# Performance work log

Measured on AMD Instinct MI355X. Metric: run time of the kernel, lower is better.

Reference implementation:

```python
import jax, jax.numpy as jnp
import numpy as np

N_NODES = 100000
N_EDGES = 3200000


def _cheb_norm(edge_index, edge_weight, num_nodes):
    # PyG ChebConv.__norm__ with normalization='sym', lambda_max=2.0:
    # L_hat = 2/lambda_max * (I - D^-1/2 A D^-1/2) - I = -D^-1/2 A D^-1/2
    # (the +1 diagonal from get_laplacian and the -1 self-loops cancel),
    # so only the off-diagonal terms -d_i^-1/2 w_ij d_j^-1/2 remain.
    src, dst = edge_index[0], edge_index[1]
    deg = jax.ops.segment_sum(edge_weight, src, num_segments=num_nodes)
    safe = jnp.where(deg > 0, deg, 1.0)
    dis = jnp.where(deg > 0, jax.lax.rsqrt(safe), 0.0)  # deg_inv_sqrt, inf -> 0
    return -dis[src] * edge_weight * dis[dst]


def _cheb_conv(x, src, dst, norm, W, b, num_nodes):
    # W: [K, C_in, C_out]. Chebyshev recurrence Tx_k = 2 L_hat Tx_{k-1} - Tx_{k-2}.
    def prop(h):  # (L_hat h)[dst] += norm_e * h[src]
        return jax.ops.segment_sum(norm[:, None] * h[src], dst, num_segments=num_nodes)

    K = W.shape[0]
    out = x @ W[0]
    if K > 1:
        tx1 = prop(x)
        out = out + tx1 @ W[1]
        if K > 2:
            def step(carry, Wk):
                tx_m2, tx_m1, acc = carry
                tx = 2.0 * prop(tx_m1) - tx_m2
                return (tx_m1, tx, acc + tx @ Wk), None
            (_, _, out), _ = jax.lax.scan(step, (x, tx1, out), W[2:])
    if b is not None:
        out = out + b
    return out


def setup_inputs() -> dict:
    key = jax.random.key(0)
    ks = jax.random.split(key, 12)
    x = jax.random.normal(ks[0], (N_NODES, 2), dtype=jnp.float32)
    edge_index = jax.random.randint(ks[1], (2, N_EDGES), 0, N_NODES, dtype=jnp.int64)
    edge_weight = jax.random.uniform(ks[2], (N_EDGES,), dtype=jnp.float32)
    s = 0.1  # keep activations in a sane range (glorot-ish scale)
    W1 = jax.random.normal(ks[3], (39, 2, 14), dtype=jnp.float32) * s
    b1 = jax.random.normal(ks[4], (14,), dtype=jnp.float32) * s
    W2 = jax.random.normal(ks[5], (43, 14, 20), dtype=jnp.float32) * s
    b2 = jax.random.normal(ks[6], (20,), dtype=jnp.float32) * s
    W3 = jax.random.normal(ks[7], (45, 20, 27), dtype=jnp.float32) * s
    b3 = jax.random.normal(ks[8], (27,), dtype=jnp.float32) * s
    W4 = jax.random.normal(ks[9], (1, 27, 1), dtype=jnp.float32) * s  # K=1, no bias
    return {"x": x, "edge_index": edge_index, "edge_weight": edge_weight,
            "W1": W1, "b1": b1, "W2": W2, "b2": b2, "W3": W3, "b3": b3, "W4": W4}


def reference(x, edge_index, edge_weight, W1, b1, W2, b2, W3, b3, W4):
    src, dst = edge_index[0], edge_index[1]
    norm = _cheb_norm(edge_index, edge_weight, N_NODES)
    h = jax.nn.silu(_cheb_conv(x, src, dst, norm, W1, b1, N_NODES))
    h = jax.nn.silu(_cheb_conv(h, src, dst, norm, W2, b2, N_NODES))
    h = jax.nn.silu(_cheb_conv(h, src, dst, norm, W3, b3, N_NODES))
    h = _cheb_conv(h, src, dst, norm, W4, None, N_NODES)
    return jax.nn.sigmoid(h)
```

## Files before the change

### kernel.cpp

```cpp
#include <hip/hip_runtime.h>
#include <math.h>

#define N_NODES 100000
#define N_EDGES 3200000
#define BS 256
#define CAP_SHIFT 7
#define CAP (1 << CAP_SHIFT)


__global__ void scan_partial_kernel(const int* __restrict__ cnt, int* __restrict__ bsums) {
    __shared__ int lds[256];
    int tid = threadIdx.x;
    int base = blockIdx.x * 1024 + tid * 4;
    int s = 0;
#pragma unroll
    for (int i = 0; i < 4; ++i) s += (base + i < N_NODES) ? cnt[base + i] : 0;
    lds[tid] = s;
    __syncthreads();
    for (int off = 128; off > 0; off >>= 1) {
        if (tid < off) lds[tid] += lds[tid + off];
        __syncthreads();
    }
    if (tid == 0) bsums[blockIdx.x] = lds[0];
}

__global__ void scan_bsums_kernel(int* __restrict__ bsums, int nb, int* __restrict__ total_out) {
    if (threadIdx.x == 0 && blockIdx.x == 0) {
        int acc = 0;
        for (int b = 0; b < nb; ++b) {
            int v = bsums[b];
            bsums[b] = acc;
            acc += v;
        }
        *total_out = acc;
    }
}

__global__ void scan_final_kernel(const int* __restrict__ cnt, const int* __restrict__ bsums,
                                  int* __restrict__ rp) {
    __shared__ int lds[256];
    int tid = threadIdx.x;
    int base = blockIdx.x * 1024 + tid * 4;
    int v[4];
    int ts = 0;
#pragma unroll
    for (int i = 0; i < 4; ++i) {
        v[i] = (base + i < N_NODES) ? cnt[base + i] : 0;
        ts += v[i];
    }
    lds[tid] = ts;
    __syncthreads();
    for (int off = 1; off < 256; off <<= 1) {
        int t = (tid >= off) ? lds[tid - off] : 0;
        __syncthreads();
        lds[tid] += t;
        __syncthreads();
    }
    int run = lds[tid] - ts + bsums[blockIdx.x];
#pragma unroll
    for (int i = 0; i < 4; ++i) {
        if (base + i < N_NODES) rp[base + i] = run;
        run += v[i];
    }
}

__global__ void fill_direct_kernel(const int* __restrict__ src, const int* __restrict__ dst,
                                   int* __restrict__ cnt_s, int* __restrict__ cnt_d,
                                   int* __restrict__ bkt_s, int* __restrict__ bkt_d) {
    int e = blockIdx.x * blockDim.x + threadIdx.x;
    if (e >= N_EDGES) return;
    int s = src[e];
    int d = dst[e];
    int slot_s = atomicAdd(&cnt_s[s], 1);
    bkt_s[((size_t)s << CAP_SHIFT) + slot_s] = e;
    int slot_d = atomicAdd(&cnt_d[d], 1);
    bkt_d[((size_t)d << CAP_SHIFT) + slot_d] = e;
}

__global__ void sort_rows_bucket_kernel(const int* __restrict__ cnt, const int* __restrict__ rp,
                                        const int* __restrict__ bkt, int* __restrict__ sorted) {
    int n = blockIdx.x * blockDim.x + threadIdx.x;
    if (n >= N_NODES) return;
    int c = cnt[n];
    const int* row = bkt + ((size_t)n << CAP_SHIFT);
    int beg = rp[n];
    for (int i = 0; i < c; ++i) {
        int v = row[i];
        int r = 0;
        for (int j = 0; j < c; ++j) r += (row[j] < v);
        sorted[beg + r] = v;
    }
}

__global__ void deg_dis_kernel(const int* __restrict__ rp_src, const int* __restrict__ sorted,
                               const float* __restrict__ w, float* __restrict__ dis) {
#pragma clang fp contract(off)
    {
        int n = blockIdx.x * blockDim.x + threadIdx.x;
        if (n >= N_NODES) return;
        float d = 0.f;
        int beg = rp_src[n], end = rp_src[n + 1];
        for (int j = beg; j < end; ++j) d = d + w[sorted[j]];
        dis[n] = (d > 0.f) ? (1.0f / sqrtf(d)) : 0.f;
    }
}

__global__ void csr_fill_kernel(const int* __restrict__ sorted, const int* __restrict__ src,
                                const int* __restrict__ dst, const float* __restrict__ w,
                                const float* __restrict__ dis, int2* __restrict__ packed) {
#pragma clang fp contract(off)
    {
        int j = blockIdx.x * blockDim.x + threadIdx.x;
        if (j >= N_EDGES) return;
        int e = sorted[j];
        int s = src[e], d = dst[e];
        float cw = ((-dis[s]) * w[e]) * dis[d];
        packed[j] = make_int2(s, __float_as_int(cw));
    }
}


template <int CIN, int COUT, int SIN, int SACC>
__global__ void layer_init_kernel(const float* __restrict__ hin, const float* __restrict__ W0,
                                  float* __restrict__ acc) {
    int t = blockIdx.x * blockDim.x + threadIdx.x;
    if (t >= N_NODES * COUT) return;
    int n = t / COUT, co = t - n * COUT;
    const float* hr = hin + (size_t)n * SIN;
    float m = 0.f;
#pragma unroll
    for (int ci = 0; ci < CIN; ++ci) m = fmaf(hr[ci], W0[ci * COUT + co], m);
    acc[(size_t)n * SACC + co] = m;
}

template <int CIN, int COUT, int SIN, int SACC, int GS, int LANES, int R>
__global__ __launch_bounds__(LANES* R) void prop_mm_kernel(
    const int* __restrict__ rp, const int2* __restrict__ pk, const float* __restrict__ hin,
    const float* __restrict__ prev, const float* __restrict__ Wk, int rec,
    float* __restrict__ tx_out, float* __restrict__ acc) {
#pragma clang fp contract(off)
    {
        __shared__ float tls[R][LANES * GS];
        int r = threadIdx.x / LANES;
        int lane = threadIdx.x - r * LANES;
        int n = blockIdx.x * R + r;
        bool vn = (n < N_NODES);
        if (vn) {
            int c0 = lane * GS;
            float s[GS];
#pragma unroll
            for (int g = 0; g < GS; ++g) s[g] = 0.f;
            int beg = rp[n], end = rp[n + 1];
            int j = beg;
            if constexpr (GS == 4) {
                for (; j + 7 < end; j += 8) {
                    int2 p0 = pk[j];
                    int2 p1 = pk[j + 1];
                    int2 p2 = pk[j + 2];
                    int2 p3 = pk[j + 3];
                    int2 p4 = pk[j + 4];
                    int2 p5 = pk[j + 5];
                    int2 p6 = pk[j + 6];
                    int2 p7 = pk[j + 7];
                    const float4 q0 = *reinterpret_cast<const float4*>(hin + (size_t)p0.x * SIN + c0);
                    const float4 q1 = *reinterpret_cast<const float4*>(hin + (size_t)p1.x * SIN + c0);
                    const float4 q2 = *reinterpret_cast<const float4*>(hin + (size_t)p2.x * SIN + c0);
                    const float4 q3 = *reinterpret_cast<const float4*>(hin + (size_t)p3.x * SIN + c0);
                    const float4 q4 = *reinterpret_cast<const float4*>(hin + (size_t)p4.x * SIN + c0);
                    const float4 q5 = *reinterpret_cast<const float4*>(hin + (size_t)p5.x * SIN + c0);
                    const float4 q6 = *reinterpret_cast<const float4*>(hin + (size_t)p6.x * SIN + c0);
                    const float4 q7 = *reinterpret_cast<const float4*>(hin + (size_t)p7.x * SIN + c0);
                    float w0 = __int_as_float(p0.y), w1 = __int_as_float(p1.y);
                    float w2 = __int_as_float(p2.y), w3 = __int_as_float(p3.y);
                    float w4 = __int_as_float(p4.y), w5 = __int_as_float(p5.y);
                    float w6 = __int_as_float(p6.y), w7 = __int_as_float(p7.y);
                    s[0] = s[0] + (w0 * q0.x); s[1] = s[1] + (w0 * q0.y);
                    s[2] = s[2] + (w0 * q0.z); s[3] = s[3] + (w0 * q0.w);
                    s[0] = s[0] + (w1 * q1.x); s[1] = s[1] + (w1 * q1.y);
                    s[2] = s[2] + (w1 * q1.z); s[3] = s[3] + (w1 * q1.w);
                    s[0] = s[0] + (w2 * q2.x); s[1] = s[1] + (w2 * q2.y);
                    s[2] = s[2] + (w2 * q2.z); s[3] = s[3] + (w2 * q2.w);
                    s[0] = s[0] + (w3 * q3.x); s[1] = s[1] + (w3 * q3.y);
                    s[2] = s[2] + (w3 * q3.z); s[3] = s[3] + (w3 * q3.w);
                    s[0] = s[0] + (w4 * q4.x); s[1] = s[1] + (w4 * q4.y);
                    s[2] = s[2] + (w4 * q4.z); s[3] = s[3] + (w4 * q4.w);
                    s[0] = s[0] + (w5 * q5.x); s[1] = s[1] + (w5 * q5.y);
                    s[2] = s[2] + (w5 * q5.z); s[3] = s[3] + (w5 * q5.w);
                    s[0] = s[0] + (w6 * q6.x); s[1] = s[1] + (w6 * q6.y);
                    s[2] = s[2] + (w6 * q6.z); s[3] = s[3] + (w6 * q6.w);
                    s[0] = s[0] + (w7 * q7.x); s[1] = s[1] + (w7 * q7.y);
                    s[2] = s[2] + (w7 * q7.z); s[3] = s[3] + (w7 * q7.w);
                }
                for (; j + 3 < end; j += 4) {
                    int2 p0 = pk[j];
                    int2 p1 = pk[j + 1];
                    int2 p2 = pk[j + 2];
                    int2 p3 = pk[j + 3];
                    const float4 q0 = *reinterpret_cast<const float4*>(hin + (size_t)p0.x * SIN + c0);
                    const float4 q1 = *reinterpret_cast<const float4*>(hin + (size_t)p1.x * SIN + c0);
                    const float4 q2 = *reinterpret_cast<const float4*>(hin + (size_t)p2.x * SIN + c0);
                    const float4 q3 = *reinterpret_cast<const float4*>(hin + (size_t)p3.x * SIN + c0);
                    float w0 = __int_as_float(p0.y), w1 = __int_as_float(p1.y);
                    float w2 = __int_as_float(p2.y), w3 = __int_as_float(p3.y);
                    s[0] = s[0] + (w0 * q0.x); s[1] = s[1] + (w0 * q0.y);
                    s[2] = s[2] + (w0 * q0.z); s[3] = s[3] + (w0 * q0.w);
                    s[0] = s[0] + (w1 * q1.x); s[1] = s[1] + (w1 * q1.y);
                    s[2] = s[2] + (w1 * q1.z); s[3] = s[3] + (w1 * q1.w);
                    s[0] = s[0] + (w2 * q2.x); s[1] = s[1] + (w2 * q2.y);
                    s[2] = s[2] + (w2 * q2.z); s[3] = s[3] + (w2 * q2.w);
                    s[0] = s[0] + (w3 * q3.x); s[1] = s[1] + (w3 * q3.y);
                    s[2] = s[2] + (w3 * q3.z); s[3] = s[3] + (w3 * q3.w);
                }
                for (; j < end; ++j) {
                    int2 p = pk[j];
                    float w = __int_as_float(p.y);
                    const float4 q = *reinterpret_cast<const float4*>(hin + (size_t)p.x * SIN + c0);
                    s[0] = s[0] + (w * q.x); s[1] = s[1] + (w * q.y);
                    s[2] = s[2] + (w * q.z); s[3] = s[3] + (w * q.w);
                }
            } else {
                for (; j + 7 < end; j += 8) {
                    int2 p0 = pk[j];
                    int2 p1 = pk[j + 1];
                    int2 p2 = pk[j + 2];
                    int2 p3 = pk[j + 3];
                    int2 p4 = pk[j + 4];
                    int2 p5 = pk[j + 5];
                    int2 p6 = pk[j + 6];
                    int2 p7 = pk[j + 7];
                    const float2 q0 = *reinterpret_cast<const float2*>(hin + (size_t)p0.x * SIN + c0);
                    const float2 q1 = *reinterpret_cast<const float2*>(hin + (size_t)p1.x * SIN + c0);
                    const float2 q2 = *reinterpret_cast<const float2*>(hin + (size_t)p2.x * SIN + c0);
                    const float2 q3 = *reinterpret_cast<const float2*>(hin + (size_t)p3.x * SIN + c0);
                    const float2 q4 = *reinterpret_cast<const float2*>(hin + (size_t)p4.x * SIN + c0);
                    const float2 q5 = *reinterpret_cast<const float2*>(hin + (size_t)p5.x * SIN + c0);
                    const float2 q6 = *reinterpret_cast<const float2*>(hin + (size_t)p6.x * SIN + c0);
                    const float2 q7 = *reinterpret_cast<const float2*>(hin + (size_t)p7.x * SIN + c0);
                    float w0 = __int_as_float(p0.y), w1 = __int_as_float(p1.y);
                    float w2 = __int_as_float(p2.y), w3 = __int_as_float(p3.y);
                    float w4 = __int_as_float(p4.y), w5 = __int_as_float(p5.y);
                    float w6 = __int_as_float(p6.y), w7 = __int_as_float(p7.y);
                    s[0] = s[0] + (w0 * q0.x); s[1] = s[1] + (w0 * q0.y);
                    s[0] = s[0] + (w1 * q1.x); s[1] = s[1] + (w1 * q1.y);
                    s[0] = s[0] + (w2 * q2.x); s[1] = s[1] + (w2 * q2.y);
                    s[0] = s[0] + (w3 * q3.x); s[1] = s[1] + (w3 * q3.y);
                    s[0] = s[0] + (w4 * q4.x); s[1] = s[1] + (w4 * q4.y);
                    s[0] = s[0] + (w5 * q5.x); s[1] = s[1] + (w5 * q5.y);
                    s[0] = s[0] + (w6 * q6.x); s[1] = s[1] + (w6 * q6.y);
                    s[0] = s[0] + (w7 * q7.x); s[1] = s[1] + (w7 * q7.y);
                }
                for (; j + 3 < end; j += 4) {
                    int2 p0 = pk[j];
                    int2 p1 = pk[j + 1];
                    int2 p2 = pk[j + 2];
                    int2 p3 = pk[j + 3];
                    const float2 q0 = *reinterpret_cast<const float2*>(hin + (size_t)p0.x * SIN + c0);
                    const float2 q1 = *reinterpret_cast<const float2*>(hin + (size_t)p1.x * SIN + c0);
                    const float2 q2 = *reinterpret_cast<const float2*>(hin + (size_t)p2.x * SIN + c0);
                    const float2 q3 = *reinterpret_cast<const float2*>(hin + (size_t)p3.x * SIN + c0);
                    float w0 = __int_as_float(p0.y), w1 = __int_as_float(p1.y);
                    float w2 = __int_as_float(p2.y), w3 = __int_as_float(p3.y);
                    s[0] = s[0] + (w0 * q0.x); s[1] = s[1] + (w0 * q0.y);
                    s[0] = s[0] + (w1 * q1.x); s[1] = s[1] + (w1 * q1.y);
                    s[0] = s[0] + (w2 * q2.x); s[1] = s[1] + (w2 * q2.y);
                    s[0] = s[0] + (w3 * q3.x); s[1] = s[1] + (w3 * q3.y);
                }
                for (; j < end; ++j) {
                    int2 p = pk[j];
                    float w = __int_as_float(p.y);
                    const float2 q = *reinterpret_cast<const float2*>(hin + (size_t)p.x * SIN + c0);
                    s[0] = s[0] + (w * q.x); s[1] = s[1] + (w * q.y);
                }
            }
            float t[GS];
            if (rec) {
#pragma unroll
                for (int g = 0; g < GS; ++g) t[g] = 2.f * s[g] - prev[(size_t)n * SIN + c0 + g];
            } else {
#pragma unroll
                for (int g = 0; g < GS; ++g) t[g] = s[g];
            }
#pragma unroll
            for (int g = 0; g < GS; ++g) tls[r][c0 + g] = t[g];
            if constexpr (GS == 4) {
                *reinterpret_cast<float4*>(tx_out + (size_t)n * SIN + c0) =
                    make_float4(t[0], t[1], t[2], t[3]);
            } else {
                *reinterpret_cast<float2*>(tx_out + (size_t)n * SIN + c0) =
                    make_float2(t[0], t[1]);
            }
        }
        __syncthreads();
        if (vn) {
            for (int co = lane; co < COUT; co += LANES) {
                float m = 0.f;
#pragma unroll
                for (int ci = 0; ci < CIN; ++ci) m = fmaf(tls[r][ci], Wk[ci * COUT + co], m);
                acc[(size_t)n * SACC + co] = acc[(size_t)n * SACC + co] + m;
            }
        }
    }
}

template <int C, int S>
__global__ void silu_bias_kernel(float* __restrict__ a, const float* __restrict__ b) {
#pragma clang fp contract(off)
    {
        int t = blockIdx.x * blockDim.x + threadIdx.x;
        if (t >= N_NODES * C) return;
        int n = t / C, c = t - n * C;
        float x = a[(size_t)n * S + c] + b[c];
        float sig = 1.f / (1.f + expf(-x));
        a[(size_t)n * S + c] = x * sig;
    }
}

__global__ void final_kernel(const float* __restrict__ h, const float* __restrict__ W4,
                             float* __restrict__ out) {
#pragma clang fp contract(off)
    {
        int n = blockIdx.x * blockDim.x + threadIdx.x;
        if (n >= N_NODES) return;
        const float* hr = h + (size_t)n * 28;
        float m = 0.f;
#pragma unroll
        for (int ci = 0; ci < 27; ++ci) m = fmaf(hr[ci], W4[ci], m);
        out[n] = 1.f / (1.f + expf(-m));
    }
}

__global__ void signal_kernel(float* __restrict__ out, float val) {
    int n = blockIdx.x * blockDim.x + threadIdx.x;
    if (n < N_NODES) out[n] = val;
}


static void run_scan(const int* cnt, int* bsums, int* rp, hipStream_t stream) {
    const int nb = (N_NODES + 1023) / 1024;
    scan_partial_kernel<<<nb, 256, 0, stream>>>(cnt, bsums);
    scan_bsums_kernel<<<1, 64, 0, stream>>>(bsums, nb, rp + N_NODES);
    scan_final_kernel<<<nb, 256, 0, stream>>>(cnt, bsums, rp);
}

template <int CIN, int COUT, int SIN, int SACC, int GS, int LANES, int R>
static void run_layer(int K, const float* hin, const float* W, float* acc, float* b0, float* b1,
                      float* b2, const int* rp, const int2* pk, hipStream_t stream) {
    const int gInit = (N_NODES * COUT + BS - 1) / BS;
    const int gProp = (N_NODES + R - 1) / R;
    layer_init_kernel<CIN, COUT, SIN, SACC><<<gInit, BS, 0, stream>>>(hin, W, acc);
    if (K > 1) {
        float* bufs[3] = {b0, b1, b2};
        prop_mm_kernel<CIN, COUT, SIN, SACC, GS, LANES, R><<<gProp, LANES * R, 0, stream>>>(
            rp, pk, hin, nullptr, W + 1 * CIN * COUT, 0, bufs[0], acc);
        const float* pm2 = hin;
        const float* pm1 = bufs[0];
        for (int k = 2; k < K; ++k) {
            float* outb = bufs[(k - 1) % 3];
            prop_mm_kernel<CIN, COUT, SIN, SACC, GS, LANES, R><<<gProp, LANES * R, 0, stream>>>(
                rp, pk, pm1, pm2, W + k * CIN * COUT, 1, outb, acc);
            pm2 = pm1;
            pm1 = outb;
        }
    }
}

extern "C" void kernel_launch(void* const* d_in, const int* in_sizes, int n_in, void* d_out,
                              int out_size, void* d_ws, size_t ws_size, hipStream_t stream) {
    const float* x  = (const float*)d_in[0];
    const int* idx  = (const int*)d_in[1];
    const float* ew = (const float*)d_in[2];
    const float* W1 = (const float*)d_in[3];
    const float* b1 = (const float*)d_in[4];
    const float* W2 = (const float*)d_in[5];
    const float* b2 = (const float*)d_in[6];
    const float* W3 = (const float*)d_in[7];
    const float* b3 = (const float*)d_in[8];
    const float* W4 = (const float*)d_in[9];
    float* out = (float*)d_out;
    (void)in_sizes; (void)n_in; (void)out_size;

    const int* src = idx;
    const int* dst = idx + N_EDGES;

    size_t off = 0;
    auto alloc = [&](size_t bytes) {
        size_t o = off;
        off = (off + bytes + 255) & ~(size_t)255;
        return o;
    };
    char* ws = (char*)d_ws;
    int*   cnt_s   = (int*)(ws + alloc(N_NODES * 4));
    int*   cnt_d   = (int*)(ws + alloc(N_NODES * 4));
    int*   rp_src  = (int*)(ws + alloc((N_NODES + 1) * 4));
    int*   rp_dst  = (int*)(ws + alloc((N_NODES + 1) * 4));
    float* dis     = (float*)(ws + alloc(N_NODES * 4));
    int*   bsums   = (int*)(ws + alloc(512));
    int2*  packed  = (int2*)(ws + alloc((size_t)N_EDGES * 8));
    const size_t pool_off = alloc(0);
    float* t0      = (float*)(ws + alloc((size_t)N_NODES * 20 * 4));
    float* t1      = (float*)(ws + alloc((size_t)N_NODES * 20 * 4));
    float* t2      = (float*)(ws + alloc((size_t)N_NODES * 20 * 4));
    float* accA    = (float*)(ws + alloc((size_t)N_NODES * 16 * 4));
    float* accB    = (float*)(ws + alloc((size_t)N_NODES * 20 * 4));
    float* accC    = (float*)(ws + alloc((size_t)N_NODES * 28 * 4));
    int*   bkt_s   = (int*)(ws + alloc((size_t)N_NODES * CAP * 4));
    int*   bkt_d   = (int*)(ws + alloc((size_t)N_NODES * CAP * 4));
    const size_t NEED = off;
    char* pool = ws + pool_off;
    int* sorted_s = (int*)(pool);
    int* sorted_d = (int*)(pool + ((size_t)16 << 20));

    int gE = (N_EDGES + BS - 1) / BS;
    int gN = (N_NODES + BS - 1) / BS;

    if (ws_size < NEED) {
        signal_kernel<<<gN, BS, 0, stream>>>(
            out, 6000.0f + (float)(ws_size / (1024.0 * 1024.0)));
        return;
    }

    (void)hipMemsetAsync(cnt_s, 0, N_NODES * 4, stream);
    (void)hipMemsetAsync(cnt_d, 0, N_NODES * 4, stream);
    fill_direct_kernel<<<gE, BS, 0, stream>>>(src, dst, cnt_s, cnt_d, bkt_s, bkt_d);
    run_scan(cnt_s, bsums, rp_src, stream);
    run_scan(cnt_d, bsums, rp_dst, stream);
    sort_rows_bucket_kernel<<<gN, BS, 0, stream>>>(cnt_s, rp_src, bkt_s, sorted_s);
    deg_dis_kernel<<<gN, BS, 0, stream>>>(rp_src, sorted_s, ew, dis);
    sort_rows_bucket_kernel<<<gN, BS, 0, stream>>>(cnt_d, rp_dst, bkt_d, sorted_d);
    csr_fill_kernel<<<gE, BS, 0, stream>>>(sorted_d, src, dst, ew, dis, packed);

    run_layer<2, 14, 2, 16, 2, 1, 256>(39, x, W1, accA, t0, t1, t2, rp_dst, packed, stream);
    silu_bias_kernel<14, 16><<<(N_NODES * 14 + BS - 1) / BS, BS, 0, stream>>>(accA, b1);
    run_layer<14, 20, 16, 20, 4, 4, 64>(43, accA, W2, accB, t0, t1, t2, rp_dst, packed, stream);
    silu_bias_kernel<20, 20><<<(N_NODES * 20 + BS - 1) / BS, BS, 0, stream>>>(accB, b2);
    run_layer<20, 27, 20, 28, 4, 5, 51>(45, accB, W3, accC, t0, t1, t2, rp_dst, packed, stream);
    silu_bias_kernel<27, 28><<<(N_NODES * 27 + BS - 1) / BS, BS, 0, stream>>>(accC, b3);
    final_kernel<<<gN, BS, 0, stream>>>(accC, W4, out);
}
```

Measured before the change: 8.148 ms.

## Fuse bucket sort with degree and CSR packing, sort rows in LDS, fuse final SiLU

Merges the per-row bucket sort with the degree/rsqrt computation and with the CSR pack step, so the intermediate sorted edge arrays are no longer written and reread. Each row (up to 64 entries) is copied into shared memory and rank-sorted there instead of repeatedly reading global memory. Rows longer than 64 fall back to a slow in-place rank search. The last bias+SiLU is folded into the final sigmoid kernel, removing one pass over the 28-wide buffer. Blocks shrink to 64 threads with large shared arrays, which may limit occupancy.

```diff
diff --git a/kernel.cpp b/kernel.cpp
--- a/kernel.cpp
+++ b/kernel.cpp
@@ -77,45 +77,89 @@
     bkt_d[((size_t)d << CAP_SHIFT) + slot_d] = e;
 }
 
-__global__ void sort_rows_bucket_kernel(const int* __restrict__ cnt, const int* __restrict__ rp,
-                                        const int* __restrict__ bkt, int* __restrict__ sorted) {
-    int n = blockIdx.x * blockDim.x + threadIdx.x;
-    if (n >= N_NODES) return;
-    int c = cnt[n];
-    const int* row = bkt + ((size_t)n << CAP_SHIFT);
-    int beg = rp[n];
-    for (int i = 0; i < c; ++i) {
-        int v = row[i];
-        int r = 0;
-        for (int j = 0; j < c; ++j) r += (row[j] < v);
-        sorted[beg + r] = v;
-    }
-}
-
-__global__ void deg_dis_kernel(const int* __restrict__ rp_src, const int* __restrict__ sorted,
-                               const float* __restrict__ w, float* __restrict__ dis) {
+__global__ __launch_bounds__(64) void sort_deg_dis_kernel(
+    const int* __restrict__ cnt, const int* __restrict__ bkt,
+    const float* __restrict__ w, float* __restrict__ dis) {
 #pragma clang fp contract(off)
     {
-        int n = blockIdx.x * blockDim.x + threadIdx.x;
+        __shared__ int lr[64][65];
+        __shared__ int ls[64][65];
+        int n = blockIdx.x * 64 + threadIdx.x;
         if (n >= N_NODES) return;
+        int c = cnt[n];
+        const int* row = bkt + ((size_t)n << CAP_SHIFT);
         float d = 0.f;
-        int beg = rp_src[n], end = rp_src[n + 1];
-        for (int j = beg; j < end; ++j) d = d + w[sorted[j]];
+        if (c <= 64) {
+            int* a = lr[threadIdx.x];
+            int* b = ls[threadIdx.x];
+            for (int i = 0; i < c; ++i) a[i] = row[i];
+            for (int i = 0; i < c; ++i) {
+                int v = a[i];
+                int rk = 0;
+                for (int j = 0; j < c; ++j) rk += (a[j] < v);
+                b[rk] = v;
+            }
+            for (int r = 0; r < c; ++r) d = d + w[b[r]];
+        } else {
+            for (int r = 0; r < c; ++r) {
+                for (int i = 0; i < c; ++i) {
+                    int v = row[i];
+                    int rk = 0;
+                    for (int j = 0; j < c; ++j) rk += (row[j] < v);
+                    if (rk == r) { d = d + w[v]; break; }
+                }
+            }
+        }
         dis[n] = (d > 0.f) ? (1.0f / sqrtf(d)) : 0.f;
     }
 }
 
-__global__ void csr_fill_kernel(const int* __restrict__ sorted, const int* __restrict__ src,
-                                const int* __restrict__ dst, const float* __restrict__ w,
-                                const float* __restrict__ dis, int2* __restrict__ packed) {
+__global__ __launch_bounds__(64) void sort_pack_kernel(
+    const int* __restrict__ cnt, const int* __restrict__ rp,
+    const int* __restrict__ bkt, const int* __restrict__ src,
+    const float* __restrict__ w, const float* __restrict__ dis,
+    int2* __restrict__ packed) {
 #pragma clang fp contract(off)
     {
-        int j = blockIdx.x * blockDim.x + threadIdx.x;
-        if (j >= N_EDGES) return;
-        int e = sorted[j];
-        int s = src[e], d = dst[e];
-        float cw = ((-dis[s]) * w[e]) * dis[d];
-        packed[j] = make_int2(s, __float_as_int(cw));
+        __shared__ int lr[64][65];
+        __shared__ int ls[64][65];
+        int n = blockIdx.x * 64 + threadIdx.x;
+        if (n >= N_NODES) return;
+        int c = cnt[n];
+        const int* row = bkt + ((size_t)n << CAP_SHIFT);
+        int beg = rp[n];
+        float din = dis[n];
+        if (c <= 64) {
+            int* a = lr[threadIdx.x];
+            int* b = ls[threadIdx.x];
+            for (int i = 0; i < c; ++i) a[i] = row[i];
+            for (int i = 0; i < c; ++i) {
+                int v = a[i];
+                int rk = 0;
+                for (int j = 0; j < c; ++j) rk += (a[j] < v);
+                b[rk] = v;
+            }
+            for (int r = 0; r < c; ++r) {
+                int e = b[r];
+                int s = src[e];
+                float cw = ((-dis[s]) * w[e]) * din;
+                packed[beg + r] = make_int2(s, __float_as_int(cw));
+            }
+        } else {
+            for (int r = 0; r < c; ++r) {
+                for (int i = 0; i < c; ++i) {
+                    int v = row[i];
+                    int rk = 0;
+                    for (int j = 0; j < c; ++j) rk += (row[j] < v);
+                    if (rk == r) {
+                        int s = src[v];
+                        float cw = ((-dis[s]) * w[v]) * din;
+                        packed[beg + r] = make_int2(s, __float_as_int(cw));
+                        break;
+                    }
+                }
+            }
+        }
     }
 }
 
@@ -315,16 +359,20 @@
     }
 }
 
-__global__ void final_kernel(const float* __restrict__ h, const float* __restrict__ W4,
-                             float* __restrict__ out) {
+__global__ void final_kernel(const float* __restrict__ acc, const float* __restrict__ b3,
+                             const float* __restrict__ W4, float* __restrict__ out) {
 #pragma clang fp contract(off)
     {
         int n = blockIdx.x * blockDim.x + threadIdx.x;
         if (n >= N_NODES) return;
-        const float* hr = h + (size_t)n * 28;
         float m = 0.f;
 #pragma unroll
-        for (int ci = 0; ci < 27; ++ci) m = fmaf(hr[ci], W4[ci], m);
+        for (int ci = 0; ci < 27; ++ci) {
+            float xv = acc[(size_t)n * 28 + ci] + b3[ci];
+            float sig = 1.f / (1.f + expf(-xv));
+            float hv = xv * sig;
+            m = fmaf(hv, W4[ci], m);
+        }
         out[n] = 1.f / (1.f + expf(-m));
     }
 }
@@ -396,7 +444,6 @@
     float* dis     = (float*)(ws + alloc(N_NODES * 4));
     int*   bsums   = (int*)(ws + alloc(512));
     int2*  packed  = (int2*)(ws + alloc((size_t)N_EDGES * 8));
-    const size_t pool_off = alloc(0);
     float* t0      = (float*)(ws + alloc((size_t)N_NODES * 20 * 4));
     float* t1      = (float*)(ws + alloc((size_t)N_NODES * 20 * 4));
     float* t2      = (float*)(ws + alloc((size_t)N_NODES * 20 * 4));
@@ -406,12 +453,10 @@
     int*   bkt_s   = (int*)(ws + alloc((size_t)N_NODES * CAP * 4));
     int*   bkt_d   = (int*)(ws + alloc((size_t)N_NODES * CAP * 4));
     const size_t NEED = off;
-    char* pool = ws + pool_off;
-    int* sorted_s = (int*)(pool);
-    int* sorted_d = (int*)(pool + ((size_t)16 << 20));
 
     int gE = (N_EDGES + BS - 1) / BS;
     int gN = (N_NODES + BS - 1) / BS;
+    const int gSort = (N_NODES + 63) / 64;
 
     if (ws_size < NEED) {
         signal_kernel<<<gN, BS, 0, stream>>>(
@@ -424,16 +469,13 @@
     fill_direct_kernel<<<gE, BS, 0, stream>>>(src, dst, cnt_s, cnt_d, bkt_s, bkt_d);
     run_scan(cnt_s, bsums, rp_src, stream);
     run_scan(cnt_d, bsums, rp_dst, stream);
-    sort_rows_bucket_kernel<<<gN, BS, 0, stream>>>(cnt_s, rp_src, bkt_s, sorted_s);
-    deg_dis_kernel<<<gN, BS, 0, stream>>>(rp_src, sorted_s, ew, dis);
-    sort_rows_bucket_kernel<<<gN, BS, 0, stream>>>(cnt_d, rp_dst, bkt_d, sorted_d);
-    csr_fill_kernel<<<gE, BS, 0, stream>>>(sorted_d, src, dst, ew, dis, packed);
+    sort_deg_dis_kernel<<<gSort, 64, 0, stream>>>(cnt_s, bkt_s, ew, dis);
+    sort_pack_kernel<<<gSort, 64, 0, stream>>>(cnt_d, rp_dst, bkt_d, src, ew, dis, packed);
 
     run_layer<2, 14, 2, 16, 2, 1, 256>(39, x, W1, accA, t0, t1, t2, rp_dst, packed, stream);
     silu_bias_kernel<14, 16><<<(N_NODES * 14 + BS - 1) / BS, BS, 0, stream>>>(accA, b1);
     run_layer<14, 20, 16, 20, 4, 4, 64>(43, accA, W2, accB, t0, t1, t2, rp_dst, packed, stream);
     silu_bias_kernel<20, 20><<<(N_NODES * 20 + BS - 1) / BS, BS, 0, stream>>>(accB, b2);
     run_layer<20, 27, 20, 28, 4, 5, 51>(45, accB, W3, accC, t0, t1, t2, rp_dst, packed, stream);
-    silu_bias_kernel<27, 28><<<(N_NODES * 27 + BS - 1) / BS, BS, 0, stream>>>(accC, b3);
-    final_kernel<<<gN, BS, 0, stream>>>(accC, W4, out);
-}
+    final_kernel<<<gN, BS, 0, stream>>>(accC, b3, W4, out);
+}
```

Result: faster. 7.692 ms (median of 2 runs) (-5.6%).
